# Kernel tuning notes

Measured on AMD Instinct MI355X. Metric: run time of the kernel, lower is better.

The kernel has to match this reference:

```python
import jax, jax.numpy as jnp
import numpy as np

DILATIONS = (1, 6, 12, 24, 36)
EPS = 1e-5


def conv2d(x, w, dil, pad):
    # x: (N,C,H,W), w: (O,I,3,3) or (O,I,1,1)
    return jax.lax.conv_general_dilated(
        x, w, window_strides=(1, 1), padding=[(pad, pad), (pad, pad)],
        rhs_dilation=(dil, dil), dimension_numbers=('NCHW', 'OIHW', 'NCHW'))


def _bilinear_sample(img, ys, xs):
    # img: (C,H,W); ys, xs: (H,W,9) float sampling coords; zero padding outside.
    C, H, W = img.shape
    y0 = jnp.floor(ys)
    x0 = jnp.floor(xs)
    wy1 = ys - y0
    wx1 = xs - x0
    wy0 = 1.0 - wy1
    wx0 = 1.0 - wx1

    def gather(yi, xi, w):
        valid = (yi >= 0) & (yi < H) & (xi >= 0) & (xi < W)
        yc = jnp.clip(yi, 0, H - 1).astype(jnp.int32)
        xc = jnp.clip(xi, 0, W - 1).astype(jnp.int32)
        v = img[:, yc, xc]  # (C,H,W,9)
        return v * (w * valid)[None]

    return (gather(y0, x0, wy0 * wx0) + gather(y0, x0 + 1, wy0 * wx1)
            + gather(y0 + 1, x0, wy1 * wx0) + gather(y0 + 1, x0 + 1, wy1 * wx1))


def deform_unfold(x, offset, dil, pad):
    # x: (N,C,H,W), offset: (N,18,H,W) interleaved (dy,dx) per 3x3 tap.
    N, C, H, W = x.shape
    ky = jnp.repeat(jnp.arange(3), 3)  # (9,)
    kx = jnp.tile(jnp.arange(3), 3)
    base_y = (jnp.arange(H)[:, None, None] + (ky * dil - pad)).astype(x.dtype)  # (H,1,9)
    base_x = (jnp.arange(W)[None, :, None] + (kx * dil - pad)).astype(x.dtype)  # (1,W,9)
    dy = jnp.transpose(offset[:, 0::2], (0, 2, 3, 1))  # (N,H,W,9)
    dx = jnp.transpose(offset[:, 1::2], (0, 2, 3, 1))
    ys = base_y[None] + dy  # (N,H,W,9)
    xs = base_x[None] + dx
    return jax.vmap(_bilinear_sample)(x, ys, xs)  # (N,C,H,W,9)


def dynamic_head(x, cat_ws, scale_w, gamma, beta):
    N, C, H, W = x.shape
    outs = [x]
    for w, dil in zip(cat_ws, DILATIONS):
        fo = conv2d(x, w, dil, dil)           # (N,27,H,W); pad == dil keeps size
        filt = jax.nn.softmax(jnp.transpose(fo[:, :9], (0, 2, 3, 1)), axis=-1)  # (N,H,W,9)
        off = fo[:, -18:]                      # (N,18,H,W)
        samp = deform_unfold(x, off, dil, dil)  # (N,C,H,W,9)
        outs.append(jnp.einsum('nchwk,nhwk->nchw', samp, filt))
    cat = jnp.concatenate(outs, axis=1)        # (N,6C,H,W)
    y = conv2d(cat, scale_w, 1, 0)             # (N,C,H,W)
    mean = jnp.mean(y, axis=(0, 2, 3))
    var = jnp.var(y, axis=(0, 2, 3))
    y = (y - mean[None, :, None, None]) * jax.lax.rsqrt(var + EPS)[None, :, None, None]
    return y * gamma[None, :, None, None] + beta[None, :, None, None]


def setup_inputs() -> dict:
    key = jax.random.key(0)
    ks = jax.random.split(key, 8)
    C = 512
    x = jax.random.normal(ks[0], (2, C, 64, 64), dtype=jnp.float32)
    cat_ws = [0.02 * jax.random.normal(ks[1 + i], (27, C, 3, 3), dtype=jnp.float32) for i in range(5)]
    scale_w = 0.02 * jax.random.normal(ks[6], (C, 6 * C, 1, 1), dtype=jnp.float32)
    gamma = jnp.ones((C,), dtype=jnp.float32)
    beta = jnp.zeros((C,), dtype=jnp.float32)
    return {'x': x, 'w1': cat_ws[0], 'w2': cat_ws[1], 'w3': cat_ws[2],
            'w4': cat_ws[3], 'w5': cat_ws[4], 'scale_w': scale_w,
            'gamma': gamma, 'beta': beta}


def reference(x, w1, w2, w3, w4, w5, scale_w, gamma, beta):
    return dynamic_head(x, (w1, w2, w3, w4, w5), scale_w, gamma, beta)
```

## Files before the change

kernel.cpp:

```cpp
#include <hip/hip_runtime.h>

typedef short short8 __attribute__((ext_vector_type(8)));
typedef float f32x4 __attribute__((ext_vector_type(4)));

#define CST 3072

__device__ __forceinline__ float bf2f(short s) {
  unsigned u = ((unsigned)(unsigned short)s) << 16;
  return __builtin_bit_cast(float, u);
}
__device__ __forceinline__ short f2bf(float f) {
  unsigned u = __builtin_bit_cast(unsigned, f);
  u = (u + 0x7FFFu + ((u >> 16) & 1u)) >> 16;
  return (short)u;
}
__device__ __forceinline__ void gl16(const short* g, short* l) {
  __builtin_amdgcn_global_load_lds(
      (const __attribute__((address_space(1))) unsigned*)g,
      (__attribute__((address_space(3))) unsigned*)l, 16, 0, 0);
}

__global__ void k_prep(const float* __restrict__ sw,
                       const float* __restrict__ w1, const float* __restrict__ w2,
                       const float* __restrict__ w3, const float* __restrict__ w4,
                       const float* __restrict__ w5,
                       short* __restrict__ wbf, short* __restrict__ wdr,
                       float* __restrict__ stats) {
  int idx = blockIdx.x * 256 + threadIdx.x;
  const int NS = 512 * 3072;
  const int NW = 5 * 9 * 32 * 512;
  if (idx < NS) {
    wbf[idx] = f2bf(sw[idx]);
  } else if (idx < NS + NW) {
    int j = idx - NS;
    int c = j & 511;
    int t2 = j >> 9;
    int oc = t2 & 31;
    int t3 = t2 >> 5;
    int tap = t3 % 9;
    int di = t3 / 9;
    float v = 0.f;
    if (oc < 27) {
      const float* wp = (di == 0) ? w1 : (di == 1) ? w2 : (di == 2) ? w3 : (di == 3) ? w4 : w5;
      v = wp[((oc * 512 + c) * 3 + tap / 3) * 3 + tap % 3];
    }
    wdr[j] = f2bf(v);
  } else if (idx < NS + NW + 1024) {
    stats[idx - NS - NW] = 0.f;
  }
}

__global__ __launch_bounds__(256) void k_transx(const float* __restrict__ x,
                                                short* __restrict__ cat) {
  __shared__ float tile[64][65];
  int b = blockIdx.x;
  int cblk = b & 7, h = (b >> 3) & 63, n = b >> 9;
  int c0 = cblk * 64;
  int t = threadIdx.x;
  int lw = t & 63, grp = t >> 6;
  const float* xp = x + (((size_t)n * 512 + c0) * 64 + h) * 64;
#pragma unroll
  for (int i = 0; i < 16; ++i) {
    int cl = grp * 16 + i;
    tile[cl][lw] = xp[(size_t)cl * 4096 + lw];
  }
  __syncthreads();
  int cl = t & 63;
  size_t mbase = ((size_t)n * 64 + h) * 64;
#pragma unroll
  for (int i = 0; i < 16; ++i) {
    int w = grp * 16 + i;
    cat[(mbase + w) * CST + c0 + cl] = f2bf(tile[cl][w]);
  }
}

__global__ __launch_bounds__(256) void k_conv(const short* __restrict__ xsrc,
                                              const short* __restrict__ wdr_all,
                                              int* __restrict__ ctab) {
  __shared__ short Bs[32][516];
  __shared__ float fo[4][16][33];
  int tid = threadIdx.x;
  int wave = tid >> 6, lane = tid & 63;
  int l15 = lane & 15, quad = lane >> 4;
  int b = blockIdx.x;
  int di = b >> 7;
  int loc = b & 127;
  int tile = (loc & 7) * 64 + (loc >> 3) * 4 + wave;
  const int DIL[5] = {1, 6, 12, 24, 36};
  int d = DIL[di];
  int m = tile * 16 + l15;
  int n = m >> 12, h = (m >> 6) & 63, w = m & 63;
  f32x4 acc0 = {0.f, 0.f, 0.f, 0.f}, acc1 = {0.f, 0.f, 0.f, 0.f};
  const short8 z8 = {0, 0, 0, 0, 0, 0, 0, 0};
#pragma unroll 1
  for (int tap = 0; tap < 9; ++tap) {
    __syncthreads();
    const short* src = wdr_all + (size_t)(di * 9 + tap) * 32 * 512;
#pragma unroll
    for (int it = 0; it < 8; ++it) {
      int chunk = it * 256 + tid;
      int oc = chunk >> 6;
      int cc = (chunk & 63) * 8;
      *(short8*)(&Bs[oc][cc]) = *(const short8*)(src + oc * 512 + cc);
    }
    __syncthreads();
    int hh = h + (tap / 3 - 1) * d;
    if ((unsigned)hh >= 64u) continue;
    int ww = w + (tap % 3 - 1) * d;
    bool ok = (unsigned)ww < 64u;
    int mrow = (n << 12) + (hh << 6) + (ok ? ww : w);
    const short* arow = xsrc + (size_t)mrow * CST + quad * 8;
#pragma unroll 4
    for (int ks = 0; ks < 16; ++ks) {
      short8 a = *(const short8*)(arow + ks * 32);
      if (!ok) a = z8;
      short8 b0 = *(const short8*)(&Bs[l15][ks * 32 + quad * 8]);
      short8 b1 = *(const short8*)(&Bs[l15 + 16][ks * 32 + quad * 8]);
      acc0 = __builtin_amdgcn_mfma_f32_16x16x32_bf16(a, b0, acc0, 0, 0, 0);
      acc1 = __builtin_amdgcn_mfma_f32_16x16x32_bf16(a, b1, acc1, 0, 0, 0);
    }
  }
#pragma unroll
  for (int r = 0; r < 4; ++r) {
    fo[wave][quad * 4 + r][l15] = acc0[r];
    fo[wave][quad * 4 + r][l15 + 16] = acc1[r];
  }
  __syncthreads();
  if (lane < 16) {
    int p = lane;
    float mx = fo[wave][p][0];
#pragma unroll
    for (int k = 1; k < 9; ++k) mx = fmaxf(mx, fo[wave][p][k]);
    float s = 0.f, e[9];
#pragma unroll
    for (int k = 0; k < 9; ++k) { e[k] = __expf(fo[wave][p][k] - mx); s += e[k]; }
    float inv = 1.f / s;
#pragma unroll
    for (int k = 0; k < 9; ++k) fo[wave][p][k] = e[k] * inv;
  }
  __syncthreads();
#pragma unroll
  for (int t3 = 0; t3 < 3; ++t3) {
    int task = t3 * 48 + lane;
    if (lane < 48) {
      int p = (task * 57) >> 9;
      int k = task - p * 9;
      float f = fo[wave][p][k];
      float dy = fo[wave][p][9 + 2 * k];
      float dx = fo[wave][p][10 + 2 * k];
      int mm = tile * 16 + p;
      int hh = (mm >> 6) & 63, ww = mm & 63;
      float ys = (float)(hh + (k / 3 - 1) * d) + dy;
      float xs = (float)(ww + (k % 3 - 1) * d) + dx;
      float y0f = floorf(ys), x0f = floorf(xs);
      float wy1 = ys - y0f, wx1 = xs - x0f;
      float wy0 = 1.f - wy1, wx0 = 1.f - wx1;
      int y0 = (int)y0f, x0 = (int)x0f;
      int4 ent;
      int* ep = (int*)&ent;
#pragma unroll
      for (int cy = 0; cy < 2; ++cy)
#pragma unroll
        for (int cx = 0; cx < 2; ++cx) {
          int yy = y0 + cy, xx = x0 + cx;
          bool v = ((unsigned)yy < 64u) && ((unsigned)xx < 64u);
          float wt = f * (cy ? wy1 : wy0) * (cx ? wx1 : wx0);
          int row = v ? (yy * 64 + xx) : 0;
          unsigned wb = v ? (unsigned)(unsigned short)f2bf(wt) : 0u;
          ep[cy * 2 + cx] = row | (int)(wb << 16);
        }
      ((int4*)ctab)[((size_t)di * 8192 + mm) * 9 + k] = ent;
    }
  }
}

__global__ __launch_bounds__(256, 4) void k_samp(const short* __restrict__ xsrc,
                                                 short* __restrict__ cat,
                                                 const int* __restrict__ ctab) {
  int tid = threadIdx.x;
  int wv = __builtin_amdgcn_readfirstlane(tid >> 6);
  int lane = tid & 63;
  int b = blockIdx.x;
  int di = b >> 11;
  int loc = b & 2047;
  int m = (loc & 7) * 1024 + (loc >> 3) * 4 + wv;
  int n = m >> 12;
  const int4* tp = (const int4*)ctab + ((size_t)di * 8192 + m) * 9;
  const short* xb = xsrc + (size_t)(n << 12) * CST + lane * 8;
  float acc[8] = {0.f, 0.f, 0.f, 0.f, 0.f, 0.f, 0.f, 0.f};
#pragma unroll
  for (int k = 0; k < 9; ++k) {
    int4 e = tp[k];
    const int* ep = (const int*)&e;
#pragma unroll
    for (int c = 0; c < 4; ++c) {
      int dw = ep[c];
      float wt = __builtin_bit_cast(float, (unsigned)dw & 0xFFFF0000u);
      int row = dw & 0xFFFF;
      const short8 vv = *(const short8*)(xb + (size_t)row * CST);
#pragma unroll
      for (int j = 0; j < 8; ++j) acc[j] += wt * bf2f(vv[j]);
    }
  }
  short8 o8;
#pragma unroll
  for (int j = 0; j < 8; ++j) o8[j] = f2bf(acc[j]);
  *(short8*)(cat + (size_t)m * CST + 512 * (di + 1) + lane * 8) = o8;
}

__global__ __launch_bounds__(256) void k_gemm(const short* __restrict__ A,
                                              const short* __restrict__ B,
                                              short* __restrict__ Y) {
  __shared__ short As[128 * 64];
  __shared__ short Bs[128 * 64];
  int tid = threadIdx.x;
  int wave = tid >> 6, lane = tid & 63;
  int l15 = lane & 15, quad = lane >> 4;
  int bid = blockIdx.x;
  int xcd = bid & 7, s = bid >> 3;
  int mt = xcd * 8 + (s >> 3);
  int nz = s & 7;
  int nt = nz & 3, kh = nz >> 2;
  int m0 = mt * 128, n0 = nt * 128;
  int kbeg = kh * 1536;
  int wm = (wave >> 1) * 64, wn = (wave & 1) * 64;
  f32x4 acc[4][4];
  f32x4 zz = {0.f, 0.f, 0.f, 0.f};
#pragma unroll
  for (int i = 0; i < 4; ++i)
#pragma unroll
    for (int j = 0; j < 4; ++j) acc[i][j] = zz;
  const short* agp[4];
  const short* bgp[4];
  short* adst[4];
  short* bdst[4];
#pragma unroll
  for (int it = 0; it < 4; ++it) {
    int q = it * 256 + tid;
    int row = q >> 3;
    int c8g = (q & 7) ^ (row & 7);
    agp[it] = A + (size_t)(m0 + row) * CST + kbeg + c8g * 8;
    bgp[it] = B + (size_t)(n0 + row) * CST + kbeg + c8g * 8;
    adst[it] = As + q * 8;
    bdst[it] = Bs + q * 8;
  }
  int slotbA = (wm + l15) & 7;
  int slotbB = (wn + l15) & 7;
#pragma unroll 1
  for (int ks = 0; ks < 24; ++ks) {
    int ko = ks * 64;
    __syncthreads();
#pragma unroll
    for (int it = 0; it < 4; ++it) gl16(agp[it] + ko, adst[it]);
#pragma unroll
    for (int it = 0; it < 4; ++it) gl16(bgp[it] + ko, bdst[it]);
    __syncthreads();
#pragma unroll
    for (int kk = 0; kk < 2; ++kk) {
      int sa = ((quad + kk * 4) ^ slotbA) * 8;
      int sb = ((quad + kk * 4) ^ slotbB) * 8;
      short8 af[4], bf[4];
#pragma unroll
      for (int i = 0; i < 4; ++i)
        af[i] = *(const short8*)(As + (wm + i * 16 + l15) * 64 + sa);
#pragma unroll
      for (int j = 0; j < 4; ++j)
        bf[j] = *(const short8*)(Bs + (wn + j * 16 + l15) * 64 + sb);
#pragma unroll
      for (int i = 0; i < 4; ++i)
#pragma unroll
        for (int j = 0; j < 4; ++j)
          acc[i][j] = __builtin_amdgcn_mfma_f32_16x16x32_bf16(af[i], bf[j], acc[i][j], 0, 0, 0);
    }
  }
  short* Yp = Y + (size_t)kh * (8192 * 512);
#pragma unroll
  for (int i = 0; i < 4; ++i) {
    int row = m0 + wm + i * 16 + quad * 4;
#pragma unroll
    for (int j = 0; j < 4; ++j) {
      int col = n0 + wn + j * 16 + l15;
#pragma unroll
      for (int r = 0; r < 4; ++r)
        Yp[(size_t)(row + r) * 512 + col] = f2bf(acc[i][j][r]);
    }
  }
}

__global__ __launch_bounds__(256) void k_stats(const short* __restrict__ Y,
                                               float* __restrict__ stats) {
  const short* Y1 = Y + (size_t)8192 * 512;
  int tid = threadIdx.x;
  int mb = blockIdx.x * 32;
  float s0 = 0.f, q0 = 0.f, s1 = 0.f, q1 = 0.f;
  for (int r = 0; r < 32; ++r) {
    size_t ro = (size_t)(mb + r) * 512;
    float v0 = bf2f(Y[ro + tid]) + bf2f(Y1[ro + tid]);
    float v1 = bf2f(Y[ro + tid + 256]) + bf2f(Y1[ro + tid + 256]);
    s0 += v0; q0 += v0 * v0;
    s1 += v1; q1 += v1 * v1;
  }
  atomicAdd(&stats[tid], s0);
  atomicAdd(&stats[tid + 256], s1);
  atomicAdd(&stats[512 + tid], q0);
  atomicAdd(&stats[512 + tid + 256], q1);
}

__global__ __launch_bounds__(256) void k_norm(const short* __restrict__ Y,
                                              const float* __restrict__ stats,
                                              const float* __restrict__ gamma,
                                              const float* __restrict__ beta,
                                              float* __restrict__ out) {
  __shared__ float tile[64][65];
  const short* Y1 = Y + (size_t)8192 * 512;
  int b = blockIdx.x;
  int cblk = b & 7, h = (b >> 3) & 63, n = b >> 9;
  int c0 = cblk * 64;
  int t = threadIdx.x;
  int cl = t & 63, grp = t >> 6;
  int c = c0 + cl;
  float mean = stats[c] * (1.f / 8192.f);
  float var = stats[512 + c] * (1.f / 8192.f) - mean * mean;
  float Ai = gamma[c] * rsqrtf(var + 1e-5f);
  float Bi = beta[c] - mean * Ai;
  size_t mbase = ((size_t)n * 64 + h) * 64;
#pragma unroll
  for (int i = 0; i < 16; ++i) {
    int w = grp * 16 + i;
    size_t ro = (mbase + w) * 512 + c;
    tile[w][cl] = (bf2f(Y[ro]) + bf2f(Y1[ro])) * Ai + Bi;
  }
  __syncthreads();
  float* op = out + (((size_t)n * 512 + c0) * 64 + h) * 64;
#pragma unroll
  for (int i = 0; i < 16; ++i) {
    int c2 = grp * 16 + i;
    op[(size_t)c2 * 4096 + cl] = tile[cl][c2];
  }
}

extern "C" void kernel_launch(void* const* d_in, const int* in_sizes, int n_in,
                              void* d_out, int out_size, void* d_ws, size_t ws_size,
                              hipStream_t stream) {
  const float* x  = (const float*)d_in[0];
  const float* w1 = (const float*)d_in[1];
  const float* w2 = (const float*)d_in[2];
  const float* w3 = (const float*)d_in[3];
  const float* w4 = (const float*)d_in[4];
  const float* w5 = (const float*)d_in[5];
  const float* sw = (const float*)d_in[6];
  const float* gamma = (const float*)d_in[7];
  const float* beta  = (const float*)d_in[8];
  float* out = (float*)d_out;

  char* ws = (char*)d_ws;
  short* cat   = (short*)ws;
  short* wbf   = (short*)(ws + 50331648);
  short* wdr   = (short*)(ws + 53477376);
  short* yb    = (short*)(ws + 54951936);
  float* stats = (float*)(ws + 71729152);
  int*   ctab  = (int*)(ws + 71733248);

  k_prep<<<9028, 256, 0, stream>>>(sw, w1, w2, w3, w4, w5, wbf, wdr, stats);
  k_transx<<<1024, 256, 0, stream>>>(x, cat);
  k_conv<<<640, 256, 0, stream>>>(cat, wdr, ctab);
  k_samp<<<10240, 256, 0, stream>>>(cat, cat, ctab);
  k_gemm<<<512, 256, 0, stream>>>(cat, wbf, yb);
  k_stats<<<256, 256, 0, stream>>>(yb, stats);
  k_norm<<<1024, 256, 0, stream>>>(yb, stats, gamma, beta, out);
}
```

Before: 238.6 us.

## Use direct global-to-LDS weight loads and prefetch A rows before barrier in offset conv

The offset-conv kernel's per-tap weight staging now uses global_load_lds DMA into a linear, ks-major LDS layout instead of register round-trips into a padded 2D array. All 16 A-row fragments for a tap are loaded into registers before the barrier, so global A loads overlap the LDS fill. Taps whose row falls outside the image now skip both the weight load and the barriers, which is safe because the skip condition is uniform across the block (each block covers one image row). The cost is more VGPRs for the 16 prefetched fragments, and possible LDS bank conflicts from the unpadded layout.

```diff
diff --git a/kernel.cpp b/kernel.cpp
--- a/kernel.cpp
+++ b/kernel.cpp
@@ -77,7 +77,7 @@
 __global__ __launch_bounds__(256) void k_conv(const short* __restrict__ xsrc,
                                               const short* __restrict__ wdr_all,
                                               int* __restrict__ ctab) {
-  __shared__ short Bs[32][516];
+  __shared__ short Bs[16384];
   __shared__ float fo[4][16][33];
   int tid = threadIdx.x;
   int wave = tid >> 6, lane = tid & 63;
@@ -85,39 +85,51 @@
   int b = blockIdx.x;
   int di = b >> 7;
   int loc = b & 127;
-  int tile = (loc & 7) * 64 + (loc >> 3) * 4 + wave;
   const int DIL[5] = {1, 6, 12, 24, 36};
   int d = DIL[di];
+  int tile4 = (loc & 7) * 16 + (loc >> 3);
+  int h = tile4 & 63, n = tile4 >> 6;
+  int tile = tile4 * 4 + wave;
   int m = tile * 16 + l15;
-  int n = m >> 12, h = (m >> 6) & 63, w = m & 63;
+  int w = m & 63;
   f32x4 acc0 = {0.f, 0.f, 0.f, 0.f}, acc1 = {0.f, 0.f, 0.f, 0.f};
   const short8 z8 = {0, 0, 0, 0, 0, 0, 0, 0};
-#pragma unroll 1
-  for (int tap = 0; tap < 9; ++tap) {
-    __syncthreads();
-    const short* src = wdr_all + (size_t)(di * 9 + tap) * 32 * 512;
-#pragma unroll
-    for (int it = 0; it < 8; ++it) {
-      int chunk = it * 256 + tid;
-      int oc = chunk >> 6;
-      int cc = (chunk & 63) * 8;
-      *(short8*)(&Bs[oc][cc]) = *(const short8*)(src + oc * 512 + cc);
-    }
-    __syncthreads();
-    int hh = h + (tap / 3 - 1) * d;
-    if ((unsigned)hh >= 64u) continue;
-    int ww = w + (tap % 3 - 1) * d;
-    bool ok = (unsigned)ww < 64u;
-    int mrow = (n << 12) + (hh << 6) + (ok ? ww : w);
-    const short* arow = xsrc + (size_t)mrow * CST + quad * 8;
-#pragma unroll 4
-    for (int ks = 0; ks < 16; ++ks) {
-      short8 a = *(const short8*)(arow + ks * 32);
-      if (!ok) a = z8;
-      short8 b0 = *(const short8*)(&Bs[l15][ks * 32 + quad * 8]);
-      short8 b1 = *(const short8*)(&Bs[l15 + 16][ks * 32 + quad * 8]);
-      acc0 = __builtin_amdgcn_mfma_f32_16x16x32_bf16(a, b0, acc0, 0, 0, 0);
-      acc1 = __builtin_amdgcn_mfma_f32_16x16x32_bf16(a, b1, acc1, 0, 0, 0);
+  int soff[8];
+  short* sdst[8];
+#pragma unroll
+  for (int it = 0; it < 8; ++it) {
+    int q = it * 256 + tid;
+    soff[it] = ((q >> 2) & 31) * 512 + (q >> 7) * 32 + (q & 3) * 8;
+    sdst[it] = Bs + q * 8;
+  }
+  const short* wbase = wdr_all + (size_t)di * 9 * 32 * 512;
+#pragma unroll
+  for (int t = 0; t < 9; ++t) {
+    int ty = t / 3, tx = t % 3;
+    int hh = h + (ty - 1) * d;
+    if ((unsigned)hh < 64u) {
+      __syncthreads();
+      const short* src = wbase + t * 32 * 512;
+#pragma unroll
+      for (int it = 0; it < 8; ++it) gl16(src + soff[it], sdst[it]);
+      int ww = w + (tx - 1) * d;
+      bool ok = (unsigned)ww < 64u;
+      int mrow = (n << 12) + (hh << 6) + (ok ? ww : w);
+      const short* arow = xsrc + (size_t)mrow * CST + quad * 8;
+      short8 a[16];
+#pragma unroll
+      for (int ks = 0; ks < 16; ++ks) {
+        short8 av = *(const short8*)(arow + ks * 32);
+        a[ks] = ok ? av : z8;
+      }
+      __syncthreads();
+#pragma unroll
+      for (int ks = 0; ks < 16; ++ks) {
+        short8 b0 = *(const short8*)(Bs + ks * 1024 + l15 * 32 + quad * 8);
+        short8 b1 = *(const short8*)(Bs + ks * 1024 + (l15 + 16) * 32 + quad * 8);
+        acc0 = __builtin_amdgcn_mfma_f32_16x16x32_bf16(a[ks], b0, acc0, 0, 0, 0);
+        acc1 = __builtin_amdgcn_mfma_f32_16x16x32_bf16(a[ks], b1, acc1, 0, 0, 0);
+      }
     }
   }
 #pragma unroll
```

Result: no change. 239.9 us (+0.6%).

## Restructure offset conv to stage full image rows in LDS with row reuse

Applied to the files above, without the earlier changes.

The dilated offset/filter conv kernel now gives each block one full 64-pixel image row. It stages that input row (256-channel halves) into swizzled LDS with async global-to-LDS loads, reuses it across the three horizontal taps, and shifts indices in LDS to apply the dilation. Before, each wave gathered A rows straight from global memory for every tap. Blocks shrink to 128 threads with 2x2 MFMA tiles per wave. The k_gemm LDS destination addressing is changed to the wave-base form that global_load_lds expects. This is likely a correctness fix there, and it trades occupancy for more LDS use.

```diff
diff --git a/kernel.cpp b/kernel.cpp
--- a/kernel.cpp
+++ b/kernel.cpp
@@ -74,84 +74,128 @@
   }
 }
 
-__global__ __launch_bounds__(256) void k_conv(const short* __restrict__ xsrc,
+__global__ __launch_bounds__(128) void k_conv(const short* __restrict__ xsrc,
                                               const short* __restrict__ wdr_all,
                                               int* __restrict__ ctab) {
-  __shared__ short Bs[32][516];
-  __shared__ float fo[4][16][33];
+  __shared__ short As[64 * 256];
+  __shared__ short Bs[32 * 256];
+  __shared__ float fo[2][32][33];
   int tid = threadIdx.x;
   int wave = tid >> 6, lane = tid & 63;
   int l15 = lane & 15, quad = lane >> 4;
   int b = blockIdx.x;
   int di = b >> 7;
   int loc = b & 127;
-  int tile = (loc & 7) * 64 + (loc >> 3) * 4 + wave;
   const int DIL[5] = {1, 6, 12, 24, 36};
   int d = DIL[di];
-  int m = tile * 16 + l15;
-  int n = m >> 12, h = (m >> 6) & 63, w = m & 63;
-  f32x4 acc0 = {0.f, 0.f, 0.f, 0.f}, acc1 = {0.f, 0.f, 0.f, 0.f};
+  int rid = (loc & 7) * 16 + (loc >> 3);
+  int h = rid & 63, n = rid >> 6;
+  f32x4 acc[2][2];
+  f32x4 zz = {0.f, 0.f, 0.f, 0.f};
+#pragma unroll
+  for (int i = 0; i < 2; ++i)
+#pragma unroll
+    for (int j = 0; j < 2; ++j) acc[i][j] = zz;
   const short8 z8 = {0, 0, 0, 0, 0, 0, 0, 0};
+  int aoff[16];
+  int boff[8];
+#pragma unroll
+  for (int i = 0; i < 16; ++i) {
+    int q = i * 128 + tid;
+    int w = q >> 5, ch = q & 31;
+    aoff[i] = w * CST + (ch ^ (w & 7)) * 8;
+  }
+#pragma unroll
+  for (int i = 0; i < 8; ++i) {
+    int q = i * 128 + tid;
+    int oc = q >> 5, ch = q & 31;
+    boff[i] = oc * 512 + (ch ^ (oc & 7)) * 8;
+  }
+  const short* wbase = wdr_all + (size_t)di * 9 * 32 * 512;
+  int rowb = (n << 12);
 #pragma unroll 1
-  for (int tap = 0; tap < 9; ++tap) {
-    __syncthreads();
-    const short* src = wdr_all + (size_t)(di * 9 + tap) * 32 * 512;
-#pragma unroll
-    for (int it = 0; it < 8; ++it) {
-      int chunk = it * 256 + tid;
-      int oc = chunk >> 6;
-      int cc = (chunk & 63) * 8;
-      *(short8*)(&Bs[oc][cc]) = *(const short8*)(src + oc * 512 + cc);
-    }
-    __syncthreads();
-    int hh = h + (tap / 3 - 1) * d;
-    if ((unsigned)hh >= 64u) continue;
-    int ww = w + (tap % 3 - 1) * d;
-    bool ok = (unsigned)ww < 64u;
-    int mrow = (n << 12) + (hh << 6) + (ok ? ww : w);
-    const short* arow = xsrc + (size_t)mrow * CST + quad * 8;
-#pragma unroll 4
-    for (int ks = 0; ks < 16; ++ks) {
-      short8 a = *(const short8*)(arow + ks * 32);
-      if (!ok) a = z8;
-      short8 b0 = *(const short8*)(&Bs[l15][ks * 32 + quad * 8]);
-      short8 b1 = *(const short8*)(&Bs[l15 + 16][ks * 32 + quad * 8]);
-      acc0 = __builtin_amdgcn_mfma_f32_16x16x32_bf16(a, b0, acc0, 0, 0, 0);
-      acc1 = __builtin_amdgcn_mfma_f32_16x16x32_bf16(a, b1, acc1, 0, 0, 0);
-    }
-  }
-#pragma unroll
-  for (int r = 0; r < 4; ++r) {
-    fo[wave][quad * 4 + r][l15] = acc0[r];
-    fo[wave][quad * 4 + r][l15 + 16] = acc1[r];
-  }
+  for (int kh = 0; kh < 2; ++kh) {
+    int lastty = -1;
+#pragma unroll
+    for (int tap = 0; tap < 9; ++tap) {
+      int ty = tap / 3, tx = tap % 3;
+      int hh = h + (ty - 1) * d;
+      if ((unsigned)hh >= 64u) continue;
+      __syncthreads();
+      if (ty != lastty) {
+        const short* abase = xsrc + (size_t)(rowb + (hh << 6)) * CST + kh * 256;
+#pragma unroll
+        for (int i = 0; i < 16; ++i)
+          gl16(abase + aoff[i], As + (i * 128 + wave * 64) * 8);
+        lastty = ty;
+      }
+      {
+        const short* bbase = wbase + tap * 32 * 512 + kh * 256;
+#pragma unroll
+        for (int i = 0; i < 8; ++i)
+          gl16(bbase + boff[i], Bs + (i * 128 + wave * 64) * 8);
+      }
+      __syncthreads();
+      int s0 = wave * 32 + (tx - 1) * d;
+#pragma unroll
+      for (int ks = 0; ks < 8; ++ks) {
+        int c = ks * 4 + quad;
+        short8 a[2], bb[2];
+#pragma unroll
+        for (int mt = 0; mt < 2; ++mt) {
+          int wp = s0 + mt * 16 + l15;
+          bool ok = (unsigned)wp < 64u;
+          int wc = ok ? wp : 0;
+          short8 av = *(const short8*)(As + wc * 256 + (c ^ (wc & 7)) * 8);
+          a[mt] = ok ? av : z8;
+        }
+#pragma unroll
+        for (int ot = 0; ot < 2; ++ot) {
+          int oc = ot * 16 + l15;
+          bb[ot] = *(const short8*)(Bs + oc * 256 + (c ^ (oc & 7)) * 8);
+        }
+#pragma unroll
+        for (int mt = 0; mt < 2; ++mt)
+#pragma unroll
+          for (int ot = 0; ot < 2; ++ot)
+            acc[mt][ot] = __builtin_amdgcn_mfma_f32_16x16x32_bf16(a[mt], bb[ot], acc[mt][ot], 0, 0, 0);
+      }
+    }
+  }
+#pragma unroll
+  for (int mt = 0; mt < 2; ++mt)
+#pragma unroll
+    for (int ot = 0; ot < 2; ++ot)
+#pragma unroll
+      for (int r = 0; r < 4; ++r)
+        fo[wave][mt * 16 + quad * 4 + r][ot * 16 + l15] = acc[mt][ot][r];
   __syncthreads();
-  if (lane < 16) {
-    int p = lane;
-    float mx = fo[wave][p][0];
-#pragma unroll
-    for (int k = 1; k < 9; ++k) mx = fmaxf(mx, fo[wave][p][k]);
+  if (tid < 64) {
+    int p = tid;
+    float* fp = fo[p >> 5][p & 31];
+    float mx = fp[0];
+#pragma unroll
+    for (int k = 1; k < 9; ++k) mx = fmaxf(mx, fp[k]);
     float s = 0.f, e[9];
 #pragma unroll
-    for (int k = 0; k < 9; ++k) { e[k] = __expf(fo[wave][p][k] - mx); s += e[k]; }
+    for (int k = 0; k < 9; ++k) { e[k] = __expf(fp[k] - mx); s += e[k]; }
     float inv = 1.f / s;
 #pragma unroll
-    for (int k = 0; k < 9; ++k) fo[wave][p][k] = e[k] * inv;
+    for (int k = 0; k < 9; ++k) fp[k] = e[k] * inv;
   }
   __syncthreads();
 #pragma unroll
-  for (int t3 = 0; t3 < 3; ++t3) {
-    int task = t3 * 48 + lane;
-    if (lane < 48) {
-      int p = (task * 57) >> 9;
+  for (int rr = 0; rr < 5; ++rr) {
+    int task = rr * 128 + tid;
+    if (task < 576) {
+      int p = task / 9;
       int k = task - p * 9;
-      float f = fo[wave][p][k];
-      float dy = fo[wave][p][9 + 2 * k];
-      float dx = fo[wave][p][10 + 2 * k];
-      int mm = tile * 16 + p;
-      int hh = (mm >> 6) & 63, ww = mm & 63;
-      float ys = (float)(hh + (k / 3 - 1) * d) + dy;
-      float xs = (float)(ww + (k % 3 - 1) * d) + dx;
+      const float* fp = fo[p >> 5][p & 31];
+      float f = fp[k];
+      float dy = fp[9 + 2 * k];
+      float dx = fp[10 + 2 * k];
+      float ys = (float)(h + (k / 3 - 1) * d) + dy;
+      float xs = (float)(p + (k % 3 - 1) * d) + dx;
       float y0f = floorf(ys), x0f = floorf(xs);
       float wy1 = ys - y0f, wx1 = xs - x0f;
       float wy0 = 1.f - wy1, wx0 = 1.f - wx1;
@@ -169,6 +213,7 @@
           unsigned wb = v ? (unsigned)(unsigned short)f2bf(wt) : 0u;
           ep[cy * 2 + cx] = row | (int)(wb << 16);
         }
+      int mm = rowb + (h << 6) + p;
       ((int4*)ctab)[((size_t)di * 8192 + mm) * 9 + k] = ent;
     }
   }
@@ -241,8 +286,8 @@
     int c8g = (q & 7) ^ (row & 7);
     agp[it] = A + (size_t)(m0 + row) * CST + kbeg + c8g * 8;
     bgp[it] = B + (size_t)(n0 + row) * CST + kbeg + c8g * 8;
-    adst[it] = As + q * 8;
-    bdst[it] = Bs + q * 8;
+    adst[it] = As + (it * 256 + (wave << 6)) * 8;
+    bdst[it] = Bs + (it * 256 + (wave << 6)) * 8;
   }
   int slotbA = (wm + l15) & 7;
   int slotbB = (wn + l15) & 7;
@@ -363,7 +408,7 @@
 
   k_prep<<<9028, 256, 0, stream>>>(sw, w1, w2, w3, w4, w5, wbf, wdr, stats);
   k_transx<<<1024, 256, 0, stream>>>(x, cat);
-  k_conv<<<640, 256, 0, stream>>>(cat, wdr, ctab);
+  k_conv<<<640, 128, 0, stream>>>(cat, wdr, ctab);
   k_samp<<<10240, 256, 0, stream>>>(cat, cat, ctab);
   k_gemm<<<512, 256, 0, stream>>>(cat, wbf, yb);
   k_stats<<<256, 256, 0, stream>>>(yb, stats);
```

Result: faster. 226.7 us (-5.0%).
